# Performance work log

Hardware: AMD Instinct MI355X
Metric: run time of the kernel (lower is better)

## Reference

```python
import jax, jax.numpy as jnp
import numpy as np

N_NODES = 50000
N_EDGES = 800000
N_S = 32          # 0e channels in node feats
N_V = 16          # 1o channels in node feats
NB = 8            # radial bessel basis size
H = 64            # MLP hidden
S_OUT = N_S + N_V           # 48 scalar message channels (filtered 0e + dot path)
V_OUT = N_V + N_S + N_V     # 64 vector message channels (filtered 1o + sxY1 + vxY2)
NUM_IRREPS = S_OUT + V_OUT  # 112, gated by radial MLP
AVG_NEIGH = 16.0


def setup_inputs() -> dict:
    key = jax.random.key(0)
    ks = jax.random.split(key, 8)
    # scale so edge lengths fall mostly inside the envelope cutoff x_max=1
    vectors = jax.random.normal(ks[0], (N_EDGES, 3), jnp.float32) * 0.25
    node_s = jax.random.normal(ks[1], (N_NODES, N_S), jnp.float32)
    node_v = jax.random.normal(ks[2], (N_NODES, N_V, 3), jnp.float32)
    senders = jax.random.randint(ks[3], (N_EDGES,), 0, N_NODES)
    receivers = jax.random.randint(ks[4], (N_EDGES,), 0, N_NODES)
    W0 = jax.random.normal(ks[5], (NB, H), jnp.float32)
    W1 = jax.random.normal(ks[6], (H, H), jnp.float32)
    W2 = jax.random.normal(ks[7], (H, NUM_IRREPS), jnp.float32)
    return {"vectors": vectors, "node_s": node_s, "node_v": node_v,
            "W0": W0, "W1": W1, "W2": W2,
            "senders": senders, "receivers": receivers}


def _radial_embed(r):
    # r: [E,1] edge lengths. Bessel basis (x_max=1) * polynomial envelope, 0 at r==0.
    n = jnp.arange(1, NB + 1, dtype=r.dtype)            # [NB]
    safe_r = jnp.maximum(r, 1e-12)
    basis = jnp.sqrt(2.0) * jnp.sin(jnp.pi * n * r) / safe_r   # [E,NB]
    x = r
    env = (1.0 - 28.0 * x**6 + 48.0 * x**7 - 21.0 * x**8) * (x < 1.0)  # smooth cutoff
    return jnp.where(r == 0.0, 0.0, basis * env)        # [E,NB]


def reference(vectors, node_s, node_v, W0, W1, W2, senders, receivers):
    E = vectors.shape[0]
    r = jnp.linalg.norm(vectors, axis=-1, keepdims=True)          # [E,1]
    u = vectors / jnp.maximum(r, 1e-12)                            # unit vectors [E,3]

    # gather sender features
    s = node_s[senders]                                            # [E,N_S]
    v = node_v[senders]                                            # [E,N_V,3]

    # equivariant tensor-product paths against spherical harmonics of u
    # (filtered to target irreps 0e,1o). Y1 ~ u, Y2 ~ traceless u u^T.
    path_a = s[:, :, None] * u[:, None, :]                         # 0e x Y1 -> 1o [E,N_S,3]
    path_b = jnp.einsum('eci,ei->ec', v, u)                        # 1o x Y1 -> 0e [E,N_V]
    T = u[:, :, None] * u[:, None, :] - jnp.eye(3, dtype=u.dtype) / 3.0  # [E,3,3]
    path_c = jnp.sqrt(1.5) * jnp.einsum('eij,ecj->eci', T, v)      # 1o x Y2 -> 1o [E,N_V,3]

    msg_s = jnp.concatenate([s, path_b], axis=-1)                  # [E,S_OUT]
    msg_v = jnp.concatenate([v, path_a, path_c], axis=1)           # [E,V_OUT,3]

    # radial MLP gate (no bias, fan-in scaled, swish hidden, linear output)
    emb = _radial_embed(r)                                         # [E,NB]
    h = jax.nn.swish(emb @ W0 / jnp.sqrt(jnp.asarray(NB, emb.dtype)))
    h = jax.nn.swish(h @ W1 / jnp.sqrt(jnp.asarray(H, emb.dtype)))
    mix = h @ W2 / jnp.sqrt(jnp.asarray(H, emb.dtype))             # [E,NUM_IRREPS]

    msg_s = msg_s * mix[:, :S_OUT]
    msg_v = msg_v * mix[:, S_OUT:, None]

    # scatter-add to receivers
    n = node_s.shape[0]
    out_s = jnp.zeros((n, S_OUT), msg_s.dtype).at[receivers].add(msg_s)
    out_v = jnp.zeros((n, V_OUT, 3), msg_v.dtype).at[receivers].add(msg_v)

    inv = 1.0 / jnp.sqrt(AVG_NEIGH)
    return jnp.concatenate([out_s * inv, (out_v * inv).reshape(n, V_OUT * 3)], axis=-1)
```

## Files before the change

kernel.cpp:

```cpp
#include <hip/hip_runtime.h>
#include <hip/hip_fp16.h>

#define N_S 32
#define N_V 16
#define NB 8
#define HH 64
#define NIR 112
#define ROW 240
#define MROW 120
#define GCAP 64

typedef _Float16 half8 __attribute__((ext_vector_type(8)));
typedef _Float16 half4v __attribute__((ext_vector_type(4)));
typedef float f32x4 __attribute__((ext_vector_type(4)));

#define H8F(arr, idx) ((float)arr[(idx) >> 3][(idx) & 7])

__device__ __forceinline__ float swishf(float x) {
  return x / (1.f + __expf(-x));
}

struct ChanDesc { int path, off, mixI, i; };

__device__ __forceinline__ void mkDesc(int t, ChanDesc& d) {
  if (t < 32) { d.path = 0; d.off = t; d.mixI = t; d.i = 0; }
  else if (t < 48) { d.path = 1; d.off = 3 * (t - 32); d.mixI = t; d.i = 0; }
  else if (t < ROW) {
    int q = t - 48, c = q / 3, i = q - 3 * c;
    d.mixI = 48 + c;
    if (c < 16) { d.path = 2; d.off = q; d.i = 0; }
    else if (c < 48) { d.path = 3; d.off = c - 16; d.i = i; }
    else { d.path = 4; d.off = 3 * (c - 48); d.i = i; }
  } else { d.path = -1; d.off = 0; d.mixI = 0; d.i = 0; }
}

__device__ __forceinline__ float evalChan(const ChanDesc& d,
                                          const float* __restrict__ srow,
                                          const float* __restrict__ vrow,
                                          float mix, float u0, float u1, float u2) {
  if (d.path < 0) return 0.f;
  if (d.path == 0) return srow[d.off] * mix;
  if (d.path == 2) return vrow[d.off] * mix;
  float uo = d.i == 0 ? u0 : (d.i == 1 ? u1 : u2);
  if (d.path == 3) return srow[d.off] * uo * mix;
  float dd = vrow[d.off] * u0 + vrow[d.off + 1] * u1 + vrow[d.off + 2] * u2;
  if (d.path == 1) return dd * mix;
  return 1.22474487139f * (uo * dd - vrow[d.off + d.i] * 0.33333333333f) * mix;
}

__device__ __forceinline__ float evalChan16(const ChanDesc& d,
                                            const _Float16* __restrict__ srow,
                                            const _Float16* __restrict__ vrow,
                                            float mix, float u0, float u1, float u2) {
  if (d.path == 0) return (float)srow[d.off] * mix;
  if (d.path == 2) return (float)vrow[d.off] * mix;
  float uo = d.i == 0 ? u0 : (d.i == 1 ? u1 : u2);
  if (d.path == 3) return (float)srow[d.off] * uo * mix;
  float dd = (float)vrow[d.off] * u0 + (float)vrow[d.off + 1] * u1 + (float)vrow[d.off + 2] * u2;
  if (d.path == 1) return dd * mix;
  return 1.22474487139f * (uo * dd - (float)vrow[d.off + d.i] * 0.33333333333f) * mix;
}

__device__ __forceinline__ void radialEmb(float x, float y, float z, bool valid,
                                          float* emb, float* u0, float* u1, float* u2) {
  float r2 = x * x + y * y + z * z;
  float r = sqrtf(r2);
  float invr = 1.f / fmaxf(r, 1e-12f);
  *u0 = x * invr; *u1 = y * invr; *u2 = z * invr;
  float env = 0.f;
  if (r < 1.f) {
    float r3 = r * r2;
    float r6 = r3 * r3;
    env = 1.f + r6 * (-28.f + (48.f - 21.f * r) * r);
  }
  float coef = 1.41421356237f * invr * env;
  if (!valid || r == 0.f) coef = 0.f;
  float ph = 3.14159265358979323846f * r;
  float s1 = __sinf(ph), c1 = __cosf(ph);
  float twc = 2.f * c1;
  float sp = 0.f, sc = s1;
#pragma unroll
  for (int n = 0; n < NB; ++n) {
    emb[n] = coef * sc;
    float sn = twc * sc - sp;
    sp = sc;
    sc = sn;
  }
}


__global__ __launch_bounds__(256) void hist_kernel(const int* __restrict__ rcv,
                                                   int* __restrict__ hist, int E) {
  int e = blockIdx.x * 256 + threadIdx.x;
  if (e < E) atomicAdd(&hist[rcv[e]], 1);
}

__global__ __launch_bounds__(256) void scan1_kernel(const int* __restrict__ hist,
                                                    int* __restrict__ scanTmp,
                                                    int* __restrict__ bsum, int N) {
  __shared__ int sh[256];
  int t = threadIdx.x;
  int i = blockIdx.x * 256 + t;
  sh[t] = (i < N) ? hist[i] : 0;
  __syncthreads();
#pragma unroll
  for (int off = 1; off < 256; off <<= 1) {
    int x = (t >= off) ? sh[t - off] : 0;
    __syncthreads();
    sh[t] += x;
    __syncthreads();
  }
  if (i < N) scanTmp[i] = sh[t];
  if (t == 255) bsum[blockIdx.x] = sh[255];
}

__global__ __launch_bounds__(256) void scan2_kernel(int* __restrict__ bsum, int nb) {
  __shared__ int sh[256];
  int t = threadIdx.x;
  sh[t] = (t < nb) ? bsum[t] : 0;
  __syncthreads();
#pragma unroll
  for (int off = 1; off < 256; off <<= 1) {
    int x = (t >= off) ? sh[t - off] : 0;
    __syncthreads();
    sh[t] += x;
    __syncthreads();
  }
  int excl = (t == 0) ? 0 : sh[t - 1];
  if (t < nb) bsum[t] = excl;
}

__global__ __launch_bounds__(256) void scan3_kernel(const int* __restrict__ scanTmp,
                                                    const int* __restrict__ bsum,
                                                    const int* __restrict__ hist,
                                                    int* __restrict__ offs,
                                                    int* __restrict__ cursor, int N) {
  int i = blockIdx.x * 256 + threadIdx.x;
  if (i < N) {
    int incl = scanTmp[i] + bsum[blockIdx.x];
    offs[i + 1] = incl;
    cursor[i] = incl - hist[i];
    if (i == 0) offs[0] = 0;
  }
}

__global__ __launch_bounds__(256) void reorderInv_kernel(const int* __restrict__ rcv,
                                                         int* __restrict__ cursor,
                                                         int* __restrict__ invPos, int E) {
  int e = blockIdx.x * 256 + threadIdx.x;
  if (e < E) {
    int pos = atomicAdd(&cursor[rcv[e]], 1);
    invPos[e] = pos;
  }
}


__global__ __launch_bounds__(256) void prep_kernel(const float* __restrict__ W1,
                                                   const float* __restrict__ W2,
                                                   const float* __restrict__ ns,
                                                   const float* __restrict__ nv,
                                                   _Float16* __restrict__ W1T,
                                                   _Float16* __restrict__ W2T,
                                                   _Float16* __restrict__ s16,
                                                   _Float16* __restrict__ v16, int N) {
  int i = blockIdx.x * 256 + threadIdx.x;
  int ts = N * N_S;
  int tv = N * N_V * 3;
  if (i < ts) s16[i] = (_Float16)ns[i];
  else if (i < ts + tv) v16[i - ts] = (_Float16)nv[i - ts];
  else if (i < ts + tv + 4096) {
    int j = i - ts - tv;
    int k = j >> 6, n = j & 63;
    W1T[n * 64 + k] = (_Float16)(W1[k * 64 + n] * 0.125f);
  } else if (i < ts + tv + 4096 + 7168) {
    int j = i - ts - tv - 4096;
    int k = j / 112, n = j - k * 112;
    W2T[n * 64 + k] = (_Float16)(W2[k * 112 + n] * 0.125f);
  }
}

__global__ __launch_bounds__(256, 2) void mlp_msg_kernel(
    const float* __restrict__ vec,
    const float* __restrict__ W0,
    const _Float16* __restrict__ W1T,
    const _Float16* __restrict__ W2T,
    const int* __restrict__ senders,
    const int* __restrict__ invPos,
    const _Float16* __restrict__ s16,
    const _Float16* __restrict__ v16,
    _Float16* __restrict__ msgS,
    int E) {
  __shared__ __align__(16) _Float16 hbuf[4 * 64 * 72];
  const int lane = threadIdx.x & 63;
  const int wave = threadIdx.x >> 6;
  const int gbase = blockIdx.x * 256 + wave * 64;
  _Float16* hb = hbuf + wave * (64 * 72);

  const int m15 = lane & 15;
  const int q = lane >> 4;

  int e = gbase + lane;
  bool valid = e < E;
  float x = 0.f, y = 0.f, z = 0.f;
  int snd = 0, pos = 0;
  if (valid) {
    const float* vp = vec + 3 * (size_t)e;
    x = vp[0]; y = vp[1]; z = vp[2];
    snd = senders[e];
    pos = invPos[e];
  }
  float emb[NB], u0, u1, u2;
  radialEmb(x, y, z, valid, emb, &u0, &u1, &u2);

  for (int kg = 0; kg < 8; ++kg) {
    half8 pk;
#pragma unroll
    for (int kk = 0; kk < 8; ++kk) {
      int k = kg * 8 + kk;
      float a = 0.f;
#pragma unroll
      for (int n = 0; n < NB; ++n) a = fmaf(emb[n], W0[n * HH + k], a);
      pk[kk] = (_Float16)swishf(a * 0.35355339059f);
    }
    *(half8*)(hb + lane * 72 + kg * 8) = pk;
  }

  half8 ss[4], vv[6];
  {
    const _Float16* sp = s16 + (size_t)snd * N_S;
    const _Float16* vp16 = v16 + (size_t)snd * (N_V * 3);
#pragma unroll
    for (int k = 0; k < 4; ++k) ss[k] = *(const half8*)(sp + k * 8);
#pragma unroll
    for (int k = 0; k < 6; ++k) vv[k] = *(const half8*)(vp16 + k * 8);
  }

  {
    half8 bW1[4][2];
#pragma unroll
    for (int nt = 0; nt < 4; ++nt)
#pragma unroll
      for (int q2 = 0; q2 < 2; ++q2)
        bW1[nt][q2] = *(const half8*)(W1T + (nt * 16 + m15) * 64 + q2 * 32 + q * 8);
#pragma unroll
    for (int t = 0; t < 4; ++t) {
      half8 a0 = *(const half8*)(hb + (t * 16 + m15) * 72 + q * 8);
      half8 a1 = *(const half8*)(hb + (t * 16 + m15) * 72 + 32 + q * 8);
#pragma unroll
      for (int nt = 0; nt < 4; ++nt) {
        f32x4 d = {0.f, 0.f, 0.f, 0.f};
        d = __builtin_amdgcn_mfma_f32_16x16x32_f16(a0, bW1[nt][0], d, 0, 0, 0);
        d = __builtin_amdgcn_mfma_f32_16x16x32_f16(a1, bW1[nt][1], d, 0, 0, 0);
#pragma unroll
        for (int r = 0; r < 4; ++r)
          hb[(t * 16 + q * 4 + r) * 72 + nt * 16 + m15] = (_Float16)swishf(d[r]);
      }
    }
  }

  half8 A2[4][2];
#pragma unroll
  for (int t = 0; t < 4; ++t)
#pragma unroll
    for (int q2 = 0; q2 < 2; ++q2)
      A2[t][q2] = *(const half8*)(hb + (t * 16 + m15) * 72 + q2 * 32 + q * 8);

  float d16[16];
#pragma unroll
  for (int j = 0; j < 16; ++j)
    d16[j] = H8F(vv, 3 * j) * u0 + H8F(vv, 3 * j + 1) * u1 + H8F(vv, 3 * j + 2) * u2;

  _Float16* orow = msgS + (size_t)pos * ROW;

  for (int nl = 0; nl < 4; ++nl) {
    half8 b0 = *(const half8*)(W2T + (nl * 16 + m15) * 64 + q * 8);
    half8 b1 = *(const half8*)(W2T + (nl * 16 + m15) * 64 + 32 + q * 8);
#pragma unroll
    for (int t = 0; t < 4; ++t) {
      f32x4 d = {0.f, 0.f, 0.f, 0.f};
      d = __builtin_amdgcn_mfma_f32_16x16x32_f16(A2[t][0], b0, d, 0, 0, 0);
      d = __builtin_amdgcn_mfma_f32_16x16x32_f16(A2[t][1], b1, d, 0, 0, 0);
#pragma unroll
      for (int r = 0; r < 4; ++r)
        hb[(t * 16 + q * 4 + r) * 72 + nl * 16 + m15] = (_Float16)d[r];
    }
  }
  half8 m0[8];
#pragma unroll
  for (int k = 0; k < 8; ++k) m0[k] = *(const half8*)(hb + lane * 72 + k * 8);

  for (int nl = 0; nl < 3; ++nl) {
    int ntg = 4 + nl;
    half8 b0 = *(const half8*)(W2T + (ntg * 16 + m15) * 64 + q * 8);
    half8 b1 = *(const half8*)(W2T + (ntg * 16 + m15) * 64 + 32 + q * 8);
#pragma unroll
    for (int t = 0; t < 4; ++t) {
      f32x4 d = {0.f, 0.f, 0.f, 0.f};
      d = __builtin_amdgcn_mfma_f32_16x16x32_f16(A2[t][0], b0, d, 0, 0, 0);
      d = __builtin_amdgcn_mfma_f32_16x16x32_f16(A2[t][1], b1, d, 0, 0, 0);
#pragma unroll
      for (int r = 0; r < 4; ++r)
        hb[(t * 16 + q * 4 + r) * 72 + nl * 16 + m15] = (_Float16)d[r];
    }
  }

#pragma unroll
  for (int ck = 0; ck < 12; ++ck) {
    half8 outv;
#pragma unroll
    for (int jj = 0; jj < 8; ++jj) {
      const int t = ck * 8 + jj;
      float val;
      if (t < 32) {
        val = H8F(m0, t) * H8F(ss, t);
      } else if (t < 48) {
        val = H8F(m0, t) * d16[t - 32];
      } else {
        const int c = (t - 48) / 3;
        val = H8F(m0, 48 + c) * H8F(vv, t - 48);
      }
      outv[jj] = (_Float16)val;
    }
    if (valid) *(half8*)(orow + ck * 8) = outv;
  }

  half8 m1[6];
#pragma unroll
  for (int k = 0; k < 6; ++k) m1[k] = *(const half8*)(hb + lane * 72 + k * 8);
#pragma unroll
  for (int ck = 0; ck < 18; ++ck) {
    half8 outv;
#pragma unroll
    for (int jj = 0; jj < 8; ++jj) {
      const int t = 96 + ck * 8 + jj;
      const int c = (t - 48) / 3;
      const int i = (t - 48) % 3;
      const float uo = (i == 0) ? u0 : ((i == 1) ? u1 : u2);
      const float m = H8F(m1, c - 16);
      float val;
      if (c < 48) {
        val = m * H8F(ss, c - 16) * uo;
      } else {
        val = 1.22474487139f * (uo * d16[c - 48] - H8F(vv, t - 192) * 0.33333333333f) * m;
      }
      outv[jj] = (_Float16)val;
    }
    if (valid) *(half8*)(orow + 96 + ck * 8) = outv;
  }
}


__global__ __launch_bounds__(256) void gather_stream_kernel(
    const _Float16* __restrict__ msgS,
    const int* __restrict__ offs,
    float* __restrict__ out, int N) {
  int wid = blockIdx.x * 4 + (threadIdx.x >> 6);
  int lane = threadIdx.x & 63;
  if (wid >= N) return;
  int s0 = __builtin_amdgcn_readfirstlane(offs[wid]);
  int s1 = __builtin_amdgcn_readfirstlane(offs[wid + 1]);
  const bool act = lane < 60;

  float a0 = 0.f, a1 = 0.f, a2 = 0.f, a3 = 0.f;
  const _Float16* base = msgS + (size_t)s0 * ROW + lane * 4;
  const int n = s1 - s0;
  int j = 0;
  for (; j + 2 <= n; j += 2) {
    half4v va = {0, 0, 0, 0}, vb = {0, 0, 0, 0};
    if (act) {
      va = *(const half4v*)(base + (size_t)j * ROW);
      vb = *(const half4v*)(base + (size_t)(j + 1) * ROW);
    }
    a0 += (float)va[0] + (float)vb[0];
    a1 += (float)va[1] + (float)vb[1];
    a2 += (float)va[2] + (float)vb[2];
    a3 += (float)va[3] + (float)vb[3];
  }
  if (j < n && act) {
    half4v va = *(const half4v*)(base + (size_t)j * ROW);
    a0 += (float)va[0]; a1 += (float)va[1]; a2 += (float)va[2]; a3 += (float)va[3];
  }
  if (act) {
    float4 o = make_float4(0.25f * a0, 0.25f * a1, 0.25f * a2, 0.25f * a3);
    *(float4*)(out + (size_t)wid * ROW + lane * 4) = o;
  }
}


__global__ __launch_bounds__(256, 4) void mlp_mfma_sorted_kernel(
    const float* __restrict__ vec,
    const float* __restrict__ W0,
    const _Float16* __restrict__ W1T,
    const _Float16* __restrict__ W2T,
    const int* __restrict__ senders,
    const int* __restrict__ invPos,
    _Float16* __restrict__ mixS,
    int E) {
  __shared__ __align__(16) _Float16 hbuf[4 * 64 * 72];
  const int lane = threadIdx.x & 63;
  const int wave = threadIdx.x >> 6;
  const int gbase = blockIdx.x * 256 + wave * 64;
  _Float16* hb = hbuf + wave * (64 * 72);

  const int m15 = lane & 15;
  const int q = lane >> 4;

  {
    int e = gbase + lane;
    bool valid = e < E;
    float x = 0.f, y = 0.f, z = 0.f;
    int snd = 0;
    if (valid) {
      const float* vp = vec + 3 * (size_t)e;
      x = vp[0]; y = vp[1]; z = vp[2];
      snd = senders[e];
    }
    float emb[NB], u0, u1, u2;
    radialEmb(x, y, z, valid, emb, &u0, &u1, &u2);
    for (int kg = 0; kg < 8; ++kg) {
      half8 pk;
#pragma unroll
      for (int kk = 0; kk < 8; ++kk) {
        int k = kg * 8 + kk;
        float a = 0.f;
#pragma unroll
        for (int n = 0; n < NB; ++n) a = fmaf(emb[n], W0[n * HH + k], a);
        pk[kk] = (_Float16)swishf(a * 0.35355339059f);
      }
      *(half8*)(hb + lane * 72 + kg * 8) = pk;
    }
    float* auxp = (float*)(hb + lane * 72 + 64);
    auxp[0] = u0; auxp[1] = u1; auxp[2] = u2;
    ((int*)auxp)[3] = snd;
  }

  half8 bW1[4][2];
#pragma unroll
  for (int nt = 0; nt < 4; ++nt)
#pragma unroll
    for (int q2 = 0; q2 < 2; ++q2)
      bW1[nt][q2] = *(const half8*)(W1T + (nt * 16 + m15) * 64 + q2 * 32 + q * 8);

#pragma unroll
  for (int t = 0; t < 4; ++t) {
    half8 a0 = *(const half8*)(hb + (t * 16 + m15) * 72 + q * 8);
    half8 a1 = *(const half8*)(hb + (t * 16 + m15) * 72 + 32 + q * 8);
#pragma unroll
    for (int nt = 0; nt < 4; ++nt) {
      f32x4 d = {0.f, 0.f, 0.f, 0.f};
      d = __builtin_amdgcn_mfma_f32_16x16x32_f16(a0, bW1[nt][0], d, 0, 0, 0);
      d = __builtin_amdgcn_mfma_f32_16x16x32_f16(a1, bW1[nt][1], d, 0, 0, 0);
#pragma unroll
      for (int r = 0; r < 4; ++r)
        hb[(t * 16 + q * 4 + r) * 72 + nt * 16 + m15] = (_Float16)swishf(d[r]);
    }
  }

  half8 A2[4][2];
#pragma unroll
  for (int t = 0; t < 4; ++t)
#pragma unroll
    for (int q2 = 0; q2 < 2; ++q2)
      A2[t][q2] = *(const half8*)(hb + (t * 16 + m15) * 72 + q2 * 32 + q * 8);

  for (int nl = 0; nl < 4; ++nl) {
    half8 b0 = *(const half8*)(W2T + (nl * 16 + m15) * 64 + q * 8);
    half8 b1 = *(const half8*)(W2T + (nl * 16 + m15) * 64 + 32 + q * 8);
#pragma unroll
    for (int t = 0; t < 4; ++t) {
      f32x4 d = {0.f, 0.f, 0.f, 0.f};
      d = __builtin_amdgcn_mfma_f32_16x16x32_f16(A2[t][0], b0, d, 0, 0, 0);
      d = __builtin_amdgcn_mfma_f32_16x16x32_f16(A2[t][1], b1, d, 0, 0, 0);
#pragma unroll
      for (int r = 0; r < 4; ++r)
        hb[(t * 16 + q * 4 + r) * 72 + nl * 16 + m15] = (_Float16)d[r];
    }
  }
  for (int it = 0; it < 8; ++it) {
    int c = it * 64 + lane;
    int el = c >> 3, p = c & 7;
    int e = gbase + el;
    half8 v = *(const half8*)(hb + el * 72 + p * 8);
    if (e < E) {
      int pos = invPos[e];
      *(half8*)(mixS + (size_t)pos * MROW + p * 8) = v;
    }
  }

  for (int nl = 0; nl < 3; ++nl) {
    int ntg = 4 + nl;
    half8 b0 = *(const half8*)(W2T + (ntg * 16 + m15) * 64 + q * 8);
    half8 b1 = *(const half8*)(W2T + (ntg * 16 + m15) * 64 + 32 + q * 8);
#pragma unroll
    for (int t = 0; t < 4; ++t) {
      f32x4 d = {0.f, 0.f, 0.f, 0.f};
      d = __builtin_amdgcn_mfma_f32_16x16x32_f16(A2[t][0], b0, d, 0, 0, 0);
      d = __builtin_amdgcn_mfma_f32_16x16x32_f16(A2[t][1], b1, d, 0, 0, 0);
#pragma unroll
      for (int r = 0; r < 4; ++r)
        hb[(t * 16 + q * 4 + r) * 72 + nl * 16 + m15] = (_Float16)d[r];
    }
  }
  for (int it = 0; it < 7; ++it) {
    int c = it * 64 + lane;
    int el = (int)(((unsigned)c * 9363u) >> 16);
    int p = c - el * 7;
    int e = gbase + el;
    half8 v = *(const half8*)(hb + el * 72 + (p < 6 ? p * 8 : 64));
    if (e < E) {
      int pos = invPos[e];
      *(half8*)(mixS + (size_t)pos * MROW + 64 + p * 8) = v;
    }
  }
}

__global__ __launch_bounds__(256) void gather_lds_kernel(
    const _Float16* __restrict__ mixS,
    const _Float16* __restrict__ s16,
    const _Float16* __restrict__ v16,
    const int* __restrict__ offs,
    float* __restrict__ out, int N) {
  __shared__ __align__(16) _Float16 mixLds[GCAP * MROW];
  __shared__ __align__(16) _Float16 nodeLds[GCAP * 80];

  const int tid = threadIdx.x;
  const int lane = tid & 63;
  const int wave = tid >> 6;
  const int wid0 = blockIdx.x * 4;

  const int e0 = offs[wid0];
  const int e4 = offs[min(wid0 + 4, N)];
  const int wid = wid0 + wave;
  const int sw = offs[min(wid, N)];
  const int ew = offs[min(wid + 1, N)];

  ChanDesc d[4];
#pragma unroll
  for (int tb = 0; tb < 4; ++tb) mkDesc(tb * 64 + lane, d[tb]);

  float acc[4] = {0.f, 0.f, 0.f, 0.f};

  for (int c0 = e0; c0 < e4; c0 += GCAP) {
    const int cnt = min(GCAP, e4 - c0);
    for (int ch = tid; ch < cnt * 15; ch += 256) {
      int row = ch / 15, part = ch - row * 15;
      *(half8*)(mixLds + row * MROW + part * 8) =
          *(const half8*)(mixS + (size_t)(c0 + row) * MROW + part * 8);
    }
    __syncthreads();
    for (int ch = tid; ch < cnt * 10; ch += 256) {
      int row = ch / 10, part = ch - row * 10;
      int snd = ((const int*)(mixLds + row * MROW + 112))[3];
      const _Float16* src = (part < 4)
          ? s16 + (size_t)snd * N_S + part * 8
          : v16 + (size_t)snd * (N_V * 3) + (part - 4) * 8;
      *(half8*)(nodeLds + row * 80 + (part < 4 ? part * 8 : 32 + (part - 4) * 8)) =
          *(const half8*)src;
    }
    __syncthreads();
    const int jlo = max(sw - c0, 0);
    const int jhi = min(ew - c0, cnt);
    for (int j = jlo; j < jhi; ++j) {
      const _Float16* row = mixLds + j * MROW;
      const float* aux = (const float*)(row + 112);
      float u0 = aux[0], u1 = aux[1], u2 = aux[2];
      const _Float16* srow = nodeLds + j * 80;
      const _Float16* vrow = srow + 32;
#pragma unroll
      for (int tb = 0; tb < 4; ++tb) {
        if (d[tb].path >= 0) {
          float m = (float)row[d[tb].mixI];
          acc[tb] += evalChan16(d[tb], srow, vrow, m, u0, u1, u2);
        }
      }
    }
    __syncthreads();
  }

  if (wid < N) {
    float* orow = out + (size_t)wid * ROW;
#pragma unroll
    for (int tb = 0; tb < 4; ++tb) {
      int t = tb * 64 + lane;
      if (t < ROW) orow[t] = 0.25f * acc[tb];
    }
  }
}


__global__ __launch_bounds__(64) void edge_kernel(
    const float* __restrict__ vec,
    const float* __restrict__ nodes_s,
    const float* __restrict__ nodes_v,
    const int* __restrict__ senders,
    const int* __restrict__ receivers,
    const float* __restrict__ W0f,
    const float* __restrict__ W1f,
    const float* __restrict__ W2f,
    float* __restrict__ out, int E) {
  __shared__ float hLds[HH * 64];
  __shared__ float uLds[64 * 3];
  __shared__ int sLds[64];
  __shared__ int rLds[64];
  __half* mixLds = reinterpret_cast<__half*>(hLds);

  const int lane = threadIdx.x;
  const int base = blockIdx.x * 64;
  const int eg = base + lane;
  const bool valid = eg < E;

  float emb[NB];
  {
    float x = 0.f, y = 0.f, z = 0.f;
    int snd = 0, rcv = 0;
    if (valid) {
      const float* vp = vec + 3 * (size_t)eg;
      x = vp[0]; y = vp[1]; z = vp[2];
      snd = senders[eg];
      rcv = receivers[eg];
    }
    float u0, u1, u2;
    radialEmb(x, y, z, valid, emb, &u0, &u1, &u2);
    uLds[lane * 3 + 0] = u0;
    uLds[lane * 3 + 1] = u1;
    uLds[lane * 3 + 2] = u2;
    sLds[lane] = snd;
    rLds[lane] = rcv;
  }

  for (int j0 = 0; j0 < HH; j0 += 8) {
    float a[8];
#pragma unroll
    for (int jj = 0; jj < 8; ++jj) a[jj] = 0.f;
#pragma unroll
    for (int k = 0; k < NB; ++k) {
      const float* wrow = W0f + k * HH + j0;
      float ek = emb[k];
#pragma unroll
      for (int jj = 0; jj < 8; ++jj) a[jj] = fmaf(ek, wrow[jj], a[jj]);
    }
#pragma unroll
    for (int jj = 0; jj < 8; ++jj)
      hLds[(j0 + jj) * 64 + lane] = swishf(a[jj] * 0.35355339059f);
  }
  __syncthreads();

  float h2[HH];
#pragma unroll
  for (int j = 0; j < HH; ++j) h2[j] = 0.f;
  for (int k = 0; k < HH; ++k) {
    float hk = hLds[k * 64 + lane];
    const float* wrow = W1f + k * HH;
#pragma unroll
    for (int j = 0; j < HH; ++j) h2[j] = fmaf(hk, wrow[j], h2[j]);
  }
#pragma unroll
  for (int j = 0; j < HH; ++j) h2[j] = swishf(h2[j] * 0.125f);
  __syncthreads();

  for (int m0 = 0; m0 < NIR; m0 += 4) {
    float a0 = 0.f, a1 = 0.f, a2 = 0.f, a3 = 0.f;
#pragma unroll
    for (int k = 0; k < HH; ++k) {
      const float* wrow = W2f + k * NIR + m0;
      float hk = h2[k];
      a0 = fmaf(hk, wrow[0], a0);
      a1 = fmaf(hk, wrow[1], a1);
      a2 = fmaf(hk, wrow[2], a2);
      a3 = fmaf(hk, wrow[3], a3);
    }
    mixLds[lane * NIR + m0 + 0] = __float2half_rn(a0 * 0.125f);
    mixLds[lane * NIR + m0 + 1] = __float2half_rn(a1 * 0.125f);
    mixLds[lane * NIR + m0 + 2] = __float2half_rn(a2 * 0.125f);
    mixLds[lane * NIR + m0 + 3] = __float2half_rn(a3 * 0.125f);
  }
  __syncthreads();

  ChanDesc d[4];
#pragma unroll
  for (int tb = 0; tb < 4; ++tb) mkDesc(tb * 64 + lane, d[tb]);

  const int cnt = min(64, E - base);
  for (int e = 0; e < cnt; ++e) {
    int snd = sLds[e], rcv = rLds[e];
    float u0 = uLds[e * 3 + 0], u1 = uLds[e * 3 + 1], u2 = uLds[e * 3 + 2];
    const float* srow = nodes_s + (size_t)snd * N_S;
    const float* vrow = nodes_v + (size_t)snd * (N_V * 3);
    const __half* mrow = mixLds + e * NIR;
    float* orow = out + (size_t)rcv * ROW;
#pragma unroll
    for (int tb = 0; tb < 4; ++tb) {
      if (d[tb].path >= 0) {
        float m = __half2float(mrow[d[tb].mixI]);
        float val = evalChan(d[tb], srow, vrow, m, u0, u1, u2);
        unsafeAtomicAdd(orow + tb * 64 + lane, 0.25f * val);
      }
    }
  }
}


extern "C" void kernel_launch(void* const* d_in, const int* in_sizes, int n_in,
                              void* d_out, int out_size, void* d_ws, size_t ws_size,
                              hipStream_t stream) {
  const float* vec = (const float*)d_in[0];
  const float* ns = (const float*)d_in[1];
  const float* nv = (const float*)d_in[2];
  const float* w0 = (const float*)d_in[3];
  const float* w1 = (const float*)d_in[4];
  const float* w2 = (const float*)d_in[5];
  const int* snd = (const int*)d_in[6];
  const int* rcv = (const int*)d_in[7];
  float* out = (float*)d_out;

  const int E = in_sizes[6];
  const int N = in_sizes[1] / N_S;
  const int nb = (N + 255) / 256;
  const int eb = (E + 255) / 256;
  const int prepElems = N * (N_S + N_V * 3) + 4096 + 7168;

  {
    char* p = (char*)d_ws;
    _Float16* msgS = (_Float16*)p;  p += (size_t)E * ROW * sizeof(_Float16);
    int* hist = (int*)p;            p += (size_t)N * 4;
    int* scanTmp = (int*)p;         p += (size_t)N * 4;
    int* offs = (int*)p;            p += ((size_t)N + 1) * 4;
    int* cursor = (int*)p;          p += (size_t)N * 4;
    int* bsum = (int*)p;            p += 256 * 4;
    int* invPos = (int*)p;          p += (size_t)E * 4;
    p = (char*)(((uintptr_t)p + 15) & ~(uintptr_t)15);
    _Float16* W1T = (_Float16*)p;   p += 4096 * sizeof(_Float16);
    _Float16* W2T = (_Float16*)p;   p += 7168 * sizeof(_Float16);
    _Float16* s16 = (_Float16*)p;   p += (size_t)N * N_S * sizeof(_Float16);
    _Float16* v16 = (_Float16*)p;   p += (size_t)N * N_V * 3 * sizeof(_Float16);
    size_t needA = (size_t)(p - (char*)d_ws);

    if (needA <= ws_size && nb <= 256) {
      hipMemsetAsync(hist, 0, (size_t)N * 4, stream);
      hist_kernel<<<eb, 256, 0, stream>>>(rcv, hist, E);
      scan1_kernel<<<nb, 256, 0, stream>>>(hist, scanTmp, bsum, N);
      scan2_kernel<<<1, 256, 0, stream>>>(bsum, nb);
      scan3_kernel<<<nb, 256, 0, stream>>>(scanTmp, bsum, hist, offs, cursor, N);
      reorderInv_kernel<<<eb, 256, 0, stream>>>(rcv, cursor, invPos, E);
      prep_kernel<<<(prepElems + 255) / 256, 256, 0, stream>>>(w1, w2, ns, nv, W1T, W2T, s16, v16, N);
      mlp_msg_kernel<<<eb, 256, 0, stream>>>(vec, w0, W1T, W2T, snd, invPos, s16, v16, msgS, E);
      gather_stream_kernel<<<(N + 3) / 4, 256, 0, stream>>>(msgS, offs, out, N);
      return;
    }
  }

  {
    char* p = (char*)d_ws;
    _Float16* mixS = (_Float16*)p;  p += (size_t)E * MROW * sizeof(_Float16);
    int* hist = (int*)p;            p += (size_t)N * 4;
    int* scanTmp = (int*)p;         p += (size_t)N * 4;
    int* offs = (int*)p;            p += ((size_t)N + 1) * 4;
    int* cursor = (int*)p;          p += (size_t)N * 4;
    int* bsum = (int*)p;            p += 256 * 4;
    int* invPos = (int*)p;          p += (size_t)E * 4;
    p = (char*)(((uintptr_t)p + 15) & ~(uintptr_t)15);
    _Float16* W1T = (_Float16*)p;   p += 4096 * sizeof(_Float16);
    _Float16* W2T = (_Float16*)p;   p += 7168 * sizeof(_Float16);
    _Float16* s16 = (_Float16*)p;   p += (size_t)N * N_S * sizeof(_Float16);
    _Float16* v16 = (_Float16*)p;   p += (size_t)N * N_V * 3 * sizeof(_Float16);
    size_t needB = (size_t)(p - (char*)d_ws);

    if (needB <= ws_size && nb <= 256) {
      hipMemsetAsync(hist, 0, (size_t)N * 4, stream);
      hist_kernel<<<eb, 256, 0, stream>>>(rcv, hist, E);
      scan1_kernel<<<nb, 256, 0, stream>>>(hist, scanTmp, bsum, N);
      scan2_kernel<<<1, 256, 0, stream>>>(bsum, nb);
      scan3_kernel<<<nb, 256, 0, stream>>>(scanTmp, bsum, hist, offs, cursor, N);
      reorderInv_kernel<<<eb, 256, 0, stream>>>(rcv, cursor, invPos, E);
      prep_kernel<<<(prepElems + 255) / 256, 256, 0, stream>>>(w1, w2, ns, nv, W1T, W2T, s16, v16, N);
      mlp_mfma_sorted_kernel<<<eb, 256, 0, stream>>>(vec, w0, W1T, W2T, snd, invPos, mixS, E);
      gather_lds_kernel<<<(N + 3) / 4, 256, 0, stream>>>(mixS, s16, v16, offs, out, N);
      return;
    }
  }

  hipMemsetAsync(d_out, 0, (size_t)out_size * sizeof(float), stream);
  edge_kernel<<<(E + 63) / 64, 64, 0, stream>>>(vec, ns, nv, snd, rcv, w0, w1, w2, out, E);
}
```

Baseline: 557.9 us.

## Fuse message compute with in-wave segmented reduction over receiver-sorted edges

Edges are now processed in receiver-sorted order, so each wave holds contiguous runs of the same receiver. The wave reduces its messages per receiver segment through LDS and writes one fp32 partial row per (node, 64-edge chunk) instead of a full fp16 message row per edge. A final gather kernel then sums the few partials per node. This removes the E×240 fp16 message buffer round trip. In exchange it adds a second scan over segment counts, many __syncthreads and serial per-segment loops in the fused kernel, and random (unsorted) reads of edge vectors and senders through the order array.

```diff
diff --git a/kernel.cpp b/kernel.cpp
--- a/kernel.cpp
+++ b/kernel.cpp
@@ -7,11 +7,8 @@
 #define HH 64
 #define NIR 112
 #define ROW 240
-#define MROW 120
-#define GCAP 64
 
 typedef _Float16 half8 __attribute__((ext_vector_type(8)));
-typedef _Float16 half4v __attribute__((ext_vector_type(4)));
 typedef float f32x4 __attribute__((ext_vector_type(4)));
 
 #define H8F(arr, idx) ((float)arr[(idx) >> 3][(idx) & 7])
@@ -48,19 +45,6 @@
   return 1.22474487139f * (uo * dd - vrow[d.off + d.i] * 0.33333333333f) * mix;
 }
 
-__device__ __forceinline__ float evalChan16(const ChanDesc& d,
-                                            const _Float16* __restrict__ srow,
-                                            const _Float16* __restrict__ vrow,
-                                            float mix, float u0, float u1, float u2) {
-  if (d.path == 0) return (float)srow[d.off] * mix;
-  if (d.path == 2) return (float)vrow[d.off] * mix;
-  float uo = d.i == 0 ? u0 : (d.i == 1 ? u1 : u2);
-  if (d.path == 3) return (float)srow[d.off] * uo * mix;
-  float dd = (float)vrow[d.off] * u0 + (float)vrow[d.off + 1] * u1 + (float)vrow[d.off + 2] * u2;
-  if (d.path == 1) return dd * mix;
-  return 1.22474487139f * (uo * dd - (float)vrow[d.off + d.i] * 0.33333333333f) * mix;
-}
-
 __device__ __forceinline__ void radialEmb(float x, float y, float z, bool valid,
                                           float* emb, float* u0, float* u1, float* u2) {
   float r2 = x * x + y * y + z * z;
@@ -144,13 +128,36 @@
   }
 }
 
-__global__ __launch_bounds__(256) void reorderInv_kernel(const int* __restrict__ rcv,
-                                                         int* __restrict__ cursor,
-                                                         int* __restrict__ invPos, int E) {
+__global__ __launch_bounds__(256) void reorderOrdR_kernel(const int* __restrict__ rcv,
+                                                          int* __restrict__ cursor,
+                                                          int* __restrict__ order,
+                                                          int* __restrict__ rcvS, int E) {
   int e = blockIdx.x * 256 + threadIdx.x;
   if (e < E) {
-    int pos = atomicAdd(&cursor[rcv[e]], 1);
-    invPos[e] = pos;
+    int rr = rcv[e];
+    int pos = atomicAdd(&cursor[rr], 1);
+    order[pos] = e;
+    rcvS[pos] = rr;
+  }
+}
+
+__global__ __launch_bounds__(256) void span_kernel(const int* __restrict__ offs,
+                                                   int* __restrict__ spanArr, int N) {
+  int i = blockIdx.x * 256 + threadIdx.x;
+  if (i < N) {
+    int s0 = offs[i], s1 = offs[i + 1];
+    spanArr[i] = (s1 > s0) ? (((s1 - 1) >> 6) - (s0 >> 6) + 1) : 0;
+  }
+}
+
+__global__ __launch_bounds__(256) void scan3seg_kernel(const int* __restrict__ scanTmp,
+                                                       const int* __restrict__ bsum,
+                                                       const int* __restrict__ spanArr,
+                                                       int* __restrict__ segStart, int N) {
+  int i = blockIdx.x * 256 + threadIdx.x;
+  if (i < N) {
+    int incl = scanTmp[i] + bsum[blockIdx.x];
+    segStart[i] = incl - spanArr[i];
   }
 }
 
@@ -179,36 +186,42 @@
   }
 }
 
-__global__ __launch_bounds__(256, 2) void mlp_msg_kernel(
+__global__ __launch_bounds__(256, 3) void fused_msg_kernel(
     const float* __restrict__ vec,
     const float* __restrict__ W0,
     const _Float16* __restrict__ W1T,
     const _Float16* __restrict__ W2T,
     const int* __restrict__ senders,
-    const int* __restrict__ invPos,
+    const int* __restrict__ order,
+    const int* __restrict__ rcvS,
+    const int* __restrict__ offs,
+    const int* __restrict__ segStart,
     const _Float16* __restrict__ s16,
     const _Float16* __restrict__ v16,
-    _Float16* __restrict__ msgS,
-    int E) {
+    float* __restrict__ partial,
+    int E, int N) {
   __shared__ __align__(16) _Float16 hbuf[4 * 64 * 72];
+  __shared__ __align__(16) float stageBuf[4 * 64 * 8];
   const int lane = threadIdx.x & 63;
   const int wave = threadIdx.x >> 6;
-  const int gbase = blockIdx.x * 256 + wave * 64;
+  const int wbase = (blockIdx.x * 4 + wave) * 64;
   _Float16* hb = hbuf + wave * (64 * 72);
+  float* stage = stageBuf + wave * (64 * 8);
 
   const int m15 = lane & 15;
   const int q = lane >> 4;
 
-  int e = gbase + lane;
-  bool valid = e < E;
+  const int pos = wbase + lane;
+  const bool valid = pos < E;
   float x = 0.f, y = 0.f, z = 0.f;
-  int snd = 0, pos = 0;
+  int snd = 0;
   if (valid) {
+    int e = order[pos];
     const float* vp = vec + 3 * (size_t)e;
     x = vp[0]; y = vp[1]; z = vp[2];
     snd = senders[e];
-    pos = invPos[e];
-  }
+  }
+  int r = valid ? rcvS[pos] : 0x7fffffff;
   float emb[NB], u0, u1, u2;
   radialEmb(x, y, z, valid, emb, &u0, &u1, &u2);
 
@@ -252,8 +265,8 @@
         d = __builtin_amdgcn_mfma_f32_16x16x32_f16(a0, bW1[nt][0], d, 0, 0, 0);
         d = __builtin_amdgcn_mfma_f32_16x16x32_f16(a1, bW1[nt][1], d, 0, 0, 0);
 #pragma unroll
-        for (int r = 0; r < 4; ++r)
-          hb[(t * 16 + q * 4 + r) * 72 + nt * 16 + m15] = (_Float16)swishf(d[r]);
+        for (int rr = 0; rr < 4; ++rr)
+          hb[(t * 16 + q * 4 + rr) * 72 + nt * 16 + m15] = (_Float16)swishf(d[rr]);
       }
     }
   }
@@ -269,8 +282,6 @@
 #pragma unroll
   for (int j = 0; j < 16; ++j)
     d16[j] = H8F(vv, 3 * j) * u0 + H8F(vv, 3 * j + 1) * u1 + H8F(vv, 3 * j + 2) * u2;
-
-  _Float16* orow = msgS + (size_t)pos * ROW;
 
   for (int nl = 0; nl < 4; ++nl) {
     half8 b0 = *(const half8*)(W2T + (nl * 16 + m15) * 64 + q * 8);
@@ -281,8 +292,8 @@
       d = __builtin_amdgcn_mfma_f32_16x16x32_f16(A2[t][0], b0, d, 0, 0, 0);
       d = __builtin_amdgcn_mfma_f32_16x16x32_f16(A2[t][1], b1, d, 0, 0, 0);
 #pragma unroll
-      for (int r = 0; r < 4; ++r)
-        hb[(t * 16 + q * 4 + r) * 72 + nl * 16 + m15] = (_Float16)d[r];
+      for (int rr = 0; rr < 4; ++rr)
+        hb[(t * 16 + q * 4 + rr) * 72 + nl * 16 + m15] = (_Float16)d[rr];
     }
   }
   half8 m0[8];
@@ -299,14 +310,47 @@
       d = __builtin_amdgcn_mfma_f32_16x16x32_f16(A2[t][0], b0, d, 0, 0, 0);
       d = __builtin_amdgcn_mfma_f32_16x16x32_f16(A2[t][1], b1, d, 0, 0, 0);
 #pragma unroll
-      for (int r = 0; r < 4; ++r)
-        hb[(t * 16 + q * 4 + r) * 72 + nl * 16 + m15] = (_Float16)d[r];
-    }
-  }
-
-#pragma unroll
+      for (int rr = 0; rr < 4; ++rr)
+        hb[(t * 16 + q * 4 + rr) * 72 + nl * 16 + m15] = (_Float16)d[rr];
+    }
+  }
+  half8 m1[6];
+#pragma unroll
+  for (int k = 0; k < 6; ++k) m1[k] = *(const half8*)(hb + lane * 72 + k * 8);
+
+  int rp = __shfl_up(r, 1);
+  bool headf = (lane == 0) || (r != rp);
+  unsigned long long mask = __ballot(headf);
+  int nseg = __popcll(mask);
+  int gsegSelf = 0;
+  if (headf && r < N)
+    gsegSelf = segStart[r] + ((wbase >> 6) - (offs[r] >> 6));
+
+  const int eo = lane >> 3;
+  const int ch = lane & 7;
+
+  auto accum = [&](int cbase) {
+    unsigned long long mm = mask;
+    for (int s = 0; s < nseg; ++s) {
+      int st = (int)__builtin_ctzll(mm);
+      mm &= mm - 1;
+      int en = mm ? (int)__builtin_ctzll(mm) : 64;
+      int node = __builtin_amdgcn_readlane(r, st);
+      if (node < N) {
+        int gs = __builtin_amdgcn_readlane(gsegSelf, st);
+        float part = 0.f;
+        for (int j = st + eo; j < en; j += 8) part += stage[j * 8 + ch];
+        part += __shfl_xor(part, 8);
+        part += __shfl_xor(part, 16);
+        part += __shfl_xor(part, 32);
+        if (eo == 0)
+          partial[(size_t)gs * ROW + cbase + ch] = part;
+      }
+    }
+  };
+
   for (int ck = 0; ck < 12; ++ck) {
-    half8 outv;
+    f32x4 o0, o1;
 #pragma unroll
     for (int jj = 0; jj < 8; ++jj) {
       const int t = ck * 8 + jj;
@@ -319,17 +363,17 @@
         const int c = (t - 48) / 3;
         val = H8F(m0, 48 + c) * H8F(vv, t - 48);
       }
-      outv[jj] = (_Float16)val;
-    }
-    if (valid) *(half8*)(orow + ck * 8) = outv;
-  }
-
-  half8 m1[6];
-#pragma unroll
-  for (int k = 0; k < 6; ++k) m1[k] = *(const half8*)(hb + lane * 72 + k * 8);
-#pragma unroll
+      if (jj < 4) o0[jj] = val; else o1[jj - 4] = val;
+    }
+    *(f32x4*)(stage + lane * 8) = o0;
+    *(f32x4*)(stage + lane * 8 + 4) = o1;
+    __syncthreads();
+    accum(ck * 8);
+    __syncthreads();
+  }
+
   for (int ck = 0; ck < 18; ++ck) {
-    half8 outv;
+    f32x4 o0, o1;
 #pragma unroll
     for (int jj = 0; jj < 8; ++jj) {
       const int t = 96 + ck * 8 + jj;
@@ -343,16 +387,20 @@
       } else {
         val = 1.22474487139f * (uo * d16[c - 48] - H8F(vv, t - 192) * 0.33333333333f) * m;
       }
-      outv[jj] = (_Float16)val;
-    }
-    if (valid) *(half8*)(orow + 96 + ck * 8) = outv;
-  }
-}
-
-
-__global__ __launch_bounds__(256) void gather_stream_kernel(
-    const _Float16* __restrict__ msgS,
+      if (jj < 4) o0[jj] = val; else o1[jj - 4] = val;
+    }
+    *(f32x4*)(stage + lane * 8) = o0;
+    *(f32x4*)(stage + lane * 8 + 4) = o1;
+    __syncthreads();
+    accum(96 + ck * 8);
+    __syncthreads();
+  }
+}
+
+__global__ __launch_bounds__(256) void gather_final_kernel(
+    const float* __restrict__ partial,
     const int* __restrict__ offs,
+    const int* __restrict__ segStart,
     float* __restrict__ out, int N) {
   int wid = blockIdx.x * 4 + (threadIdx.x >> 6);
   int lane = threadIdx.x & 63;
@@ -361,229 +409,18 @@
   int s1 = __builtin_amdgcn_readfirstlane(offs[wid + 1]);
   const bool act = lane < 60;
 
-  float a0 = 0.f, a1 = 0.f, a2 = 0.f, a3 = 0.f;
-  const _Float16* base = msgS + (size_t)s0 * ROW + lane * 4;
-  const int n = s1 - s0;
-  int j = 0;
-  for (; j + 2 <= n; j += 2) {
-    half4v va = {0, 0, 0, 0}, vb = {0, 0, 0, 0};
-    if (act) {
-      va = *(const half4v*)(base + (size_t)j * ROW);
-      vb = *(const half4v*)(base + (size_t)(j + 1) * ROW);
-    }
-    a0 += (float)va[0] + (float)vb[0];
-    a1 += (float)va[1] + (float)vb[1];
-    a2 += (float)va[2] + (float)vb[2];
-    a3 += (float)va[3] + (float)vb[3];
-  }
-  if (j < n && act) {
-    half4v va = *(const half4v*)(base + (size_t)j * ROW);
-    a0 += (float)va[0]; a1 += (float)va[1]; a2 += (float)va[2]; a3 += (float)va[3];
+  f32x4 acc = {0.f, 0.f, 0.f, 0.f};
+  if (s1 > s0) {
+    int k0 = __builtin_amdgcn_readfirstlane(segStart[wid]);
+    int nsg = ((s1 - 1) >> 6) - (s0 >> 6) + 1;
+    const float* base = partial + (size_t)k0 * ROW + lane * 4;
+    for (int j = 0; j < nsg; ++j) {
+      if (act) acc += *(const f32x4*)(base + (size_t)j * ROW);
+    }
   }
   if (act) {
-    float4 o = make_float4(0.25f * a0, 0.25f * a1, 0.25f * a2, 0.25f * a3);
-    *(float4*)(out + (size_t)wid * ROW + lane * 4) = o;
-  }
-}
-
-
-__global__ __launch_bounds__(256, 4) void mlp_mfma_sorted_kernel(
-    const float* __restrict__ vec,
-    const float* __restrict__ W0,
-    const _Float16* __restrict__ W1T,
-    const _Float16* __restrict__ W2T,
-    const int* __restrict__ senders,
-    const int* __restrict__ invPos,
-    _Float16* __restrict__ mixS,
-    int E) {
-  __shared__ __align__(16) _Float16 hbuf[4 * 64 * 72];
-  const int lane = threadIdx.x & 63;
-  const int wave = threadIdx.x >> 6;
-  const int gbase = blockIdx.x * 256 + wave * 64;
-  _Float16* hb = hbuf + wave * (64 * 72);
-
-  const int m15 = lane & 15;
-  const int q = lane >> 4;
-
-  {
-    int e = gbase + lane;
-    bool valid = e < E;
-    float x = 0.f, y = 0.f, z = 0.f;
-    int snd = 0;
-    if (valid) {
-      const float* vp = vec + 3 * (size_t)e;
-      x = vp[0]; y = vp[1]; z = vp[2];
-      snd = senders[e];
-    }
-    float emb[NB], u0, u1, u2;
-    radialEmb(x, y, z, valid, emb, &u0, &u1, &u2);
-    for (int kg = 0; kg < 8; ++kg) {
-      half8 pk;
-#pragma unroll
-      for (int kk = 0; kk < 8; ++kk) {
-        int k = kg * 8 + kk;
-        float a = 0.f;
-#pragma unroll
-        for (int n = 0; n < NB; ++n) a = fmaf(emb[n], W0[n * HH + k], a);
-        pk[kk] = (_Float16)swishf(a * 0.35355339059f);
-      }
-      *(half8*)(hb + lane * 72 + kg * 8) = pk;
-    }
-    float* auxp = (float*)(hb + lane * 72 + 64);
-    auxp[0] = u0; auxp[1] = u1; auxp[2] = u2;
-    ((int*)auxp)[3] = snd;
-  }
-
-  half8 bW1[4][2];
-#pragma unroll
-  for (int nt = 0; nt < 4; ++nt)
-#pragma unroll
-    for (int q2 = 0; q2 < 2; ++q2)
-      bW1[nt][q2] = *(const half8*)(W1T + (nt * 16 + m15) * 64 + q2 * 32 + q * 8);
-
-#pragma unroll
-  for (int t = 0; t < 4; ++t) {
-    half8 a0 = *(const half8*)(hb + (t * 16 + m15) * 72 + q * 8);
-    half8 a1 = *(const half8*)(hb + (t * 16 + m15) * 72 + 32 + q * 8);
-#pragma unroll
-    for (int nt = 0; nt < 4; ++nt) {
-      f32x4 d = {0.f, 0.f, 0.f, 0.f};
-      d = __builtin_amdgcn_mfma_f32_16x16x32_f16(a0, bW1[nt][0], d, 0, 0, 0);
-      d = __builtin_amdgcn_mfma_f32_16x16x32_f16(a1, bW1[nt][1], d, 0, 0, 0);
-#pragma unroll
-      for (int r = 0; r < 4; ++r)
-        hb[(t * 16 + q * 4 + r) * 72 + nt * 16 + m15] = (_Float16)swishf(d[r]);
-    }
-  }
-
-  half8 A2[4][2];
-#pragma unroll
-  for (int t = 0; t < 4; ++t)
-#pragma unroll
-    for (int q2 = 0; q2 < 2; ++q2)
-      A2[t][q2] = *(const half8*)(hb + (t * 16 + m15) * 72 + q2 * 32 + q * 8);
-
-  for (int nl = 0; nl < 4; ++nl) {
-    half8 b0 = *(const half8*)(W2T + (nl * 16 + m15) * 64 + q * 8);
-    half8 b1 = *(const half8*)(W2T + (nl * 16 + m15) * 64 + 32 + q * 8);
-#pragma unroll
-    for (int t = 0; t < 4; ++t) {
-      f32x4 d = {0.f, 0.f, 0.f, 0.f};
-      d = __builtin_amdgcn_mfma_f32_16x16x32_f16(A2[t][0], b0, d, 0, 0, 0);
-      d = __builtin_amdgcn_mfma_f32_16x16x32_f16(A2[t][1], b1, d, 0, 0, 0);
-#pragma unroll
-      for (int r = 0; r < 4; ++r)
-        hb[(t * 16 + q * 4 + r) * 72 + nl * 16 + m15] = (_Float16)d[r];
-    }
-  }
-  for (int it = 0; it < 8; ++it) {
-    int c = it * 64 + lane;
-    int el = c >> 3, p = c & 7;
-    int e = gbase + el;
-    half8 v = *(const half8*)(hb + el * 72 + p * 8);
-    if (e < E) {
-      int pos = invPos[e];
-      *(half8*)(mixS + (size_t)pos * MROW + p * 8) = v;
-    }
-  }
-
-  for (int nl = 0; nl < 3; ++nl) {
-    int ntg = 4 + nl;
-    half8 b0 = *(const half8*)(W2T + (ntg * 16 + m15) * 64 + q * 8);
-    half8 b1 = *(const half8*)(W2T + (ntg * 16 + m15) * 64 + 32 + q * 8);
-#pragma unroll
-    for (int t = 0; t < 4; ++t) {
-      f32x4 d = {0.f, 0.f, 0.f, 0.f};
-      d = __builtin_amdgcn_mfma_f32_16x16x32_f16(A2[t][0], b0, d, 0, 0, 0);
-      d = __builtin_amdgcn_mfma_f32_16x16x32_f16(A2[t][1], b1, d, 0, 0, 0);
-#pragma unroll
-      for (int r = 0; r < 4; ++r)
-        hb[(t * 16 + q * 4 + r) * 72 + nl * 16 + m15] = (_Float16)d[r];
-    }
-  }
-  for (int it = 0; it < 7; ++it) {
-    int c = it * 64 + lane;
-    int el = (int)(((unsigned)c * 9363u) >> 16);
-    int p = c - el * 7;
-    int e = gbase + el;
-    half8 v = *(const half8*)(hb + el * 72 + (p < 6 ? p * 8 : 64));
-    if (e < E) {
-      int pos = invPos[e];
-      *(half8*)(mixS + (size_t)pos * MROW + 64 + p * 8) = v;
-    }
-  }
-}
-
-__global__ __launch_bounds__(256) void gather_lds_kernel(
-    const _Float16* __restrict__ mixS,
-    const _Float16* __restrict__ s16,
-    const _Float16* __restrict__ v16,
-    const int* __restrict__ offs,
-    float* __restrict__ out, int N) {
-  __shared__ __align__(16) _Float16 mixLds[GCAP * MROW];
-  __shared__ __align__(16) _Float16 nodeLds[GCAP * 80];
-
-  const int tid = threadIdx.x;
-  const int lane = tid & 63;
-  const int wave = tid >> 6;
-  const int wid0 = blockIdx.x * 4;
-
-  const int e0 = offs[wid0];
-  const int e4 = offs[min(wid0 + 4, N)];
-  const int wid = wid0 + wave;
-  const int sw = offs[min(wid, N)];
-  const int ew = offs[min(wid + 1, N)];
-
-  ChanDesc d[4];
-#pragma unroll
-  for (int tb = 0; tb < 4; ++tb) mkDesc(tb * 64 + lane, d[tb]);
-
-  float acc[4] = {0.f, 0.f, 0.f, 0.f};
-
-  for (int c0 = e0; c0 < e4; c0 += GCAP) {
-    const int cnt = min(GCAP, e4 - c0);
-    for (int ch = tid; ch < cnt * 15; ch += 256) {
-      int row = ch / 15, part = ch - row * 15;
-      *(half8*)(mixLds + row * MROW + part * 8) =
-          *(const half8*)(mixS + (size_t)(c0 + row) * MROW + part * 8);
-    }
-    __syncthreads();
-    for (int ch = tid; ch < cnt * 10; ch += 256) {
-      int row = ch / 10, part = ch - row * 10;
-      int snd = ((const int*)(mixLds + row * MROW + 112))[3];
-      const _Float16* src = (part < 4)
-          ? s16 + (size_t)snd * N_S + part * 8
-          : v16 + (size_t)snd * (N_V * 3) + (part - 4) * 8;
-      *(half8*)(nodeLds + row * 80 + (part < 4 ? part * 8 : 32 + (part - 4) * 8)) =
-          *(const half8*)src;
-    }
-    __syncthreads();
-    const int jlo = max(sw - c0, 0);
-    const int jhi = min(ew - c0, cnt);
-    for (int j = jlo; j < jhi; ++j) {
-      const _Float16* row = mixLds + j * MROW;
-      const float* aux = (const float*)(row + 112);
-      float u0 = aux[0], u1 = aux[1], u2 = aux[2];
-      const _Float16* srow = nodeLds + j * 80;
-      const _Float16* vrow = srow + 32;
-#pragma unroll
-      for (int tb = 0; tb < 4; ++tb) {
-        if (d[tb].path >= 0) {
-          float m = (float)row[d[tb].mixI];
-          acc[tb] += evalChan16(d[tb], srow, vrow, m, u0, u1, u2);
-        }
-      }
-    }
-    __syncthreads();
-  }
-
-  if (wid < N) {
-    float* orow = out + (size_t)wid * ROW;
-#pragma unroll
-    for (int tb = 0; tb < 4; ++tb) {
-      int t = tb * 64 + lane;
-      if (t < ROW) orow[t] = 0.25f * acc[tb];
-    }
+    f32x4 o = 0.25f * acc;
+    *(f32x4*)(out + (size_t)wid * ROW + lane * 4) = o;
   }
 }
 
@@ -720,61 +557,40 @@
   const int prepElems = N * (N_S + N_V * 3) + 4096 + 7168;
 
   {
+    const size_t segCap = (size_t)N + (size_t)E / 64 + 256;
     char* p = (char*)d_ws;
-    _Float16* msgS = (_Float16*)p;  p += (size_t)E * ROW * sizeof(_Float16);
     int* hist = (int*)p;            p += (size_t)N * 4;
     int* scanTmp = (int*)p;         p += (size_t)N * 4;
     int* offs = (int*)p;            p += ((size_t)N + 1) * 4;
     int* cursor = (int*)p;          p += (size_t)N * 4;
+    int* segStart = (int*)p;        p += (size_t)N * 4;
     int* bsum = (int*)p;            p += 256 * 4;
-    int* invPos = (int*)p;          p += (size_t)E * 4;
+    int* order = (int*)p;           p += (size_t)E * 4;
+    int* rcvS = (int*)p;            p += (size_t)E * 4;
     p = (char*)(((uintptr_t)p + 15) & ~(uintptr_t)15);
     _Float16* W1T = (_Float16*)p;   p += 4096 * sizeof(_Float16);
     _Float16* W2T = (_Float16*)p;   p += 7168 * sizeof(_Float16);
     _Float16* s16 = (_Float16*)p;   p += (size_t)N * N_S * sizeof(_Float16);
     _Float16* v16 = (_Float16*)p;   p += (size_t)N * N_V * 3 * sizeof(_Float16);
-    size_t needA = (size_t)(p - (char*)d_ws);
-
-    if (needA <= ws_size && nb <= 256) {
+    p = (char*)(((uintptr_t)p + 15) & ~(uintptr_t)15);
+    float* partial = (float*)p;     p += segCap * ROW * sizeof(float);
+    size_t need = (size_t)(p - (char*)d_ws);
+
+    if (need <= ws_size && nb <= 256) {
       hipMemsetAsync(hist, 0, (size_t)N * 4, stream);
       hist_kernel<<<eb, 256, 0, stream>>>(rcv, hist, E);
       scan1_kernel<<<nb, 256, 0, stream>>>(hist, scanTmp, bsum, N);
       scan2_kernel<<<1, 256, 0, stream>>>(bsum, nb);
       scan3_kernel<<<nb, 256, 0, stream>>>(scanTmp, bsum, hist, offs, cursor, N);
-      reorderInv_kernel<<<eb, 256, 0, stream>>>(rcv, cursor, invPos, E);
-      prep_kernel<<<(prepElems + 255) / 256, 256, 0, stream>>>(w1, w2, ns, nv, W1T, W2T, s16, v16, N);
-      mlp_msg_kernel<<<eb, 256, 0, stream>>>(vec, w0, W1T, W2T, snd, invPos, s16, v16, msgS, E);
-      gather_stream_kernel<<<(N + 3) / 4, 256, 0, stream>>>(msgS, offs, out, N);
-      return;
-    }
-  }
-
-  {
-    char* p = (char*)d_ws;
-    _Float16* mixS = (_Float16*)p;  p += (size_t)E * MROW * sizeof(_Float16);
-    int* hist = (int*)p;            p += (size_t)N * 4;
-    int* scanTmp = (int*)p;         p += (size_t)N * 4;
-    int* offs = (int*)p;            p += ((size_t)N + 1) * 4;
-    int* cursor = (int*)p;          p += (size_t)N * 4;
-    int* bsum = (int*)p;            p += 256 * 4;
-    int* invPos = (int*)p;          p += (size_t)E * 4;
-    p = (char*)(((uintptr_t)p + 15) & ~(uintptr_t)15);
-    _Float16* W1T = (_Float16*)p;   p += 4096 * sizeof(_Float16);
-    _Float16* W2T = (_Float16*)p;   p += 7168 * sizeof(_Float16);
-    _Float16* s16 = (_Float16*)p;   p += (size_t)N * N_S * sizeof(_Float16);
-    _Float16* v16 = (_Float16*)p;   p += (size_t)N * N_V * 3 * sizeof(_Float16);
-    size_t needB = (size_t)(p - (char*)d_ws);
-
-    if (needB <= ws_size && nb <= 256) {
-      hipMemsetAsync(hist, 0, (size_t)N * 4, stream);
-      hist_kernel<<<eb, 256, 0, stream>>>(rcv, hist, E);
+      reorderOrdR_kernel<<<eb, 256, 0, stream>>>(rcv, cursor, order, rcvS, E);
+      span_kernel<<<nb, 256, 0, stream>>>(offs, hist, N);
       scan1_kernel<<<nb, 256, 0, stream>>>(hist, scanTmp, bsum, N);
       scan2_kernel<<<1, 256, 0, stream>>>(bsum, nb);
-      scan3_kernel<<<nb, 256, 0, stream>>>(scanTmp, bsum, hist, offs, cursor, N);
-      reorderInv_kernel<<<eb, 256, 0, stream>>>(rcv, cursor, invPos, E);
+      scan3seg_kernel<<<nb, 256, 0, stream>>>(scanTmp, bsum, hist, segStart, N);
       prep_kernel<<<(prepElems + 255) / 256, 256, 0, stream>>>(w1, w2, ns, nv, W1T, W2T, s16, v16, N);
-      mlp_mfma_sorted_kernel<<<eb, 256, 0, stream>>>(vec, w0, W1T, W2T, snd, invPos, mixS, E);
-      gather_lds_kernel<<<(N + 3) / 4, 256, 0, stream>>>(mixS, s16, v16, offs, out, N);
+      fused_msg_kernel<<<eb, 256, 0, stream>>>(vec, w0, W1T, W2T, snd, order, rcvS,
+                                               offs, segStart, s16, v16, partial, E, N);
+      gather_final_kernel<<<(N + 3) / 4, 256, 0, stream>>>(partial, offs, segStart, out, N);
       return;
     }
   }
```

Result: slower. 1.027 ms (+84.1%).
